# Kernel tuning notes

Hardware: AMD Instinct MI355X
Metric: run time of the kernel (lower is better)

The kernel has to match this reference:

```python
import jax, jax.numpy as jnp
import numpy as np

K_SIZE = 5      # kernel_size
NUM_ITERS = 3   # num_iters
EPS = 1e-6


def _unfold(x, k):
    """Mimic F.unfold(x, k, padding=k//2) -> (B, N, K, D) with K=k*k, N=H*W.
    Channel ordering matches torch: unfold gives (B, D*K, N) with d-major, so
    view(B, D, K, N).permute(0, 3, 2, 1) == transpose below."""
    B, D, H, W = x.shape
    p = k // 2
    xp = jnp.pad(x, ((0, 0), (0, 0), (p, p), (p, p)))
    # stack k*k shifted views -> (B, D, K, H, W); loop is over the fixed 5x5 window
    patches = jnp.stack([xp[:, :, i:i + H, j:j + W]
                         for i in range(k) for j in range(k)], axis=2)
    return patches.reshape(B, D, k * k, H * W).transpose(0, 3, 2, 1)  # (B,N,K,D)


def setup_inputs() -> dict:
    key = jax.random.key(0)
    embeddings = jax.random.normal(key, (2, 32, 256, 256), dtype=jnp.float32)
    # init_bandwidth=1.0 -> log(exp(1)-1) so softplus(log_bandwidth)=1.0
    log_bandwidth = jnp.asarray(np.log(np.exp(1.0) - 1.0), dtype=jnp.float32)
    return {"embeddings": embeddings, "log_bandwidth": log_bandwidth}


def reference(embeddings, log_bandwidth):
    B, D, H, W = embeddings.shape
    N = H * W
    z = embeddings.reshape(B, D, N).transpose(0, 2, 1)  # (B, N, D)
    bandwidth = jax.nn.softplus(log_bandwidth)
    inv_2bw2 = 1.0 / (2.0 * bandwidth * bandwidth)
    # NOTE: original code unfolds `embeddings` (not z) every iter -> constant patches
    patches = _unfold(embeddings, K_SIZE)  # (B, N, K, D)
    for _ in range(NUM_ITERS):
        z_flat = jax.lax.stop_gradient(z)  # matches z.detach()
        diff = patches - z_flat[:, :, None, :]           # (B, N, K, D)
        dist2 = jnp.sum(diff * diff, axis=-1)            # (B, N, K)
        weights = jnp.exp(-dist2 * inv_2bw2)             # gaussian kernel
        numerator = jnp.einsum('bnk,bnkd->bnd', weights, patches)
        denom = jnp.sum(weights, axis=2, keepdims=True) + EPS
        z = numerator / denom
    # default flags: only shifted embeddings are returned
    return z.transpose(0, 2, 1).reshape(B, D, H, W)
```

## Files before the change

### kernel.cpp

```cpp
#include <hip/hip_runtime.h>
#include <math.h>


typedef _Float16 h2  __attribute__((ext_vector_type(2)));
typedef _Float16 h8  __attribute__((ext_vector_type(8)));
typedef unsigned int u4v __attribute__((ext_vector_type(4)));

constexpr int Dch  = 32;
constexpr int HH   = 256;
constexpr int WW   = 256;
constexpr int PADp = 2;
constexpr int BH   = 16;
constexpr int BW   = 16;
constexpr int TH   = BH + 2 * PADp;
constexpr int TWd  = BW + 2 * PADp;
constexpr int NPIX = TH * TWd;
constexpr int NPIXP = 402;
constexpr int NCHK = 4;
constexpr int ITERS = 3;
constexpr int HWp  = HH * WW;
constexpr int NTHR = 512;

__device__ __forceinline__ float fdot2f(h2 a, h2 b, float c) {
    return __builtin_amdgcn_fdot2(a, b, c, false);
}

__device__ __forceinline__ float EXP2F(float x) {
#if __has_builtin(__builtin_amdgcn_exp2f)
    return __builtin_amdgcn_exp2f(x);
#else
    return __expf(x * 0.69314718055994531f);
#endif
}

__device__ __forceinline__ float qswap(float x) {
#if __has_builtin(__builtin_amdgcn_mov_dpp)
    return __int_as_float(
        __builtin_amdgcn_mov_dpp(__float_as_int(x), 0xB1, 0xF, 0xF, true));
#else
    return __shfl_xor(x, 1, 64);
#endif
}

__device__ __forceinline__ h2 as_h2(unsigned int x) {
    return __builtin_bit_cast(h2, x);
}

__global__ __launch_bounds__(NTHR, 4)
void meanshift_kernel(const float* __restrict__ E,
                      const float* __restrict__ lbw,
                      float* __restrict__ out)
{
    __shared__ u4v tile[NCHK][NPIXP];

    const int b    = blockIdx.z;
    const int oh   = blockIdx.y * BH - PADp;
    const int ow   = blockIdx.x * BW - PADp;
    const int tid  = threadIdx.x;
    const int half = tid & 1;
    const int pix  = tid >> 1;
    const int px   = pix & (BW - 1);
    const int py   = pix >> 4;
    const int c0   = 2 * half;

    const float bwv   = log1pf(__expf(lbw[0]));
    const float cc2   = 1.0f / (2.0f * bwv * bwv);
    const float negNC = -cc2 * 1.44269504f;

    const float* Eb = E + (size_t)b * Dch * HWp;

    for (int job = tid; job < NCHK * NPIX; job += NTHR) {
        const int cc = job / NPIX;
        const int p  = job - cc * NPIX;
        const int tr = p / TWd;
        const int tc = p - tr * TWd;
        const int gh = oh + tr;
        const int gw = ow + tc;
        h8 v;
        if ((unsigned)gh < (unsigned)HH && (unsigned)gw < (unsigned)WW) {
            const float* p0 = Eb + (size_t)(8 * cc) * HWp + gh * WW + gw;
            #pragma unroll
            for (int k = 0; k < 8; ++k) v[k] = (_Float16)p0[k * HWp];
        } else {
            #pragma unroll
            for (int k = 0; k < 8; ++k) v[k] = (_Float16)0.f;
        }
        tile[cc][p] = __builtin_bit_cast(u4v, v);
    }
    __syncthreads();

    const u4v* __restrict__ tA = tile[c0];
    const u4v* __restrict__ tB = tile[c0 + 1];

    const int myp = (py + PADp) * TWd + (px + PADp);
    h2 z0, z1, z2, z3, z4, z5, z6, z7;
    {
        const u4v ca = tA[myp];
        const u4v cb = tB[myp];
        z0 = as_h2(ca[0]); z1 = as_h2(ca[1]); z2 = as_h2(ca[2]); z3 = as_h2(ca[3]);
        z4 = as_h2(cb[0]); z5 = as_h2(cb[1]); z6 = as_h2(cb[2]); z7 = as_h2(cb[3]);
    }

    float* Ob = out + (size_t)b * Dch * HWp;
    const int off    = (oh + PADp + py) * WW + (ow + PADp + px);
    const int chbase = 16 * half;

#define NBODY(NPI) do {                                                       \
        const u4v a  = tA[(NPI)];                                             \
        const u4v bq = tB[(NPI)];                                             \
        const h2 pa0 = as_h2(a[0]),  pa1 = as_h2(a[1]);                       \
        const h2 pa2 = as_h2(a[2]),  pa3 = as_h2(a[3]);                       \
        const h2 pb0 = as_h2(bq[0]), pb1 = as_h2(bq[1]);                      \
        const h2 pb2 = as_h2(bq[2]), pb3 = as_h2(bq[3]);                      \
        const h2 e0 = pa0 - z0, e1 = pa1 - z1, e2 = pa2 - z2, e3 = pa3 - z3;  \
        const h2 f0 = pb0 - z4, f1 = pb1 - z5, f2 = pb2 - z6, f3 = pb3 - z7;  \
        float s0 = fdot2f(e0, e0, 0.f);                                       \
        s0 = fdot2f(e1, e1, s0); s0 = fdot2f(e2, e2, s0);                     \
        s0 = fdot2f(e3, e3, s0);                                              \
        float s1 = fdot2f(f0, f0, 0.f);                                       \
        s1 = fdot2f(f1, f1, s1); s1 = fdot2f(f2, f2, s1);                     \
        s1 = fdot2f(f3, f3, s1);                                              \
        const float dp   = s0 + s1;                                           \
        const float dist = dp + qswap(dp);                                    \
        const float w    = EXP2F(dist * negNC);                               \
        den += w;                                                             \
        const _Float16 wh = (_Float16)w;                                      \
        const h2 w2v = {wh, wh};                                              \
        n0 += pa0 * w2v; n1 += pa1 * w2v; n2 += pa2 * w2v; n3 += pa3 * w2v;   \
        n4 += pb0 * w2v; n5 += pb1 * w2v; n6 += pb2 * w2v; n7 += pb3 * w2v;   \
    } while (0)

    #pragma unroll 1
    for (int it = 0; it < ITERS; ++it) {
        h2 n0 = {(_Float16)0.f, (_Float16)0.f};
        h2 n1 = n0, n2 = n0, n3 = n0, n4 = n0, n5 = n0, n6 = n0, n7 = n0;
        float den = 0.f;

        #pragma unroll 1
        for (int di = 0; di < 5; ++di) {
            const int rb = (py + di) * TWd + px;
            NBODY(rb + 0);
            NBODY(rb + 1);
            NBODY(rb + 2);
            NBODY(rb + 3);
            NBODY(rb + 4);
        }

        const float invf = 1.0f / (den + 1e-6f);
        if (it == ITERS - 1) {
#define WR(IDX, NV, EL) Ob[(size_t)(chbase + (IDX)) * HWp + off] = (float)NV[EL] * invf
            WR(0,  n0, 0); WR(1,  n0, 1); WR(2,  n1, 0); WR(3,  n1, 1);
            WR(4,  n2, 0); WR(5,  n2, 1); WR(6,  n3, 0); WR(7,  n3, 1);
            WR(8,  n4, 0); WR(9,  n4, 1); WR(10, n5, 0); WR(11, n5, 1);
            WR(12, n6, 0); WR(13, n6, 1); WR(14, n7, 0); WR(15, n7, 1);
#undef WR
        } else {
            const _Float16 ih = (_Float16)invf;
            const h2 iv = {ih, ih};
            z0 = n0 * iv; z1 = n1 * iv; z2 = n2 * iv; z3 = n3 * iv;
            z4 = n4 * iv; z5 = n5 * iv; z6 = n6 * iv; z7 = n7 * iv;
        }
    }
#undef NBODY
}

extern "C" void kernel_launch(void* const* d_in, const int* in_sizes, int n_in,
                              void* d_out, int out_size, void* d_ws, size_t ws_size,
                              hipStream_t stream) {
    const float* E   = (const float*)d_in[0];
    const float* lbw = (const float*)d_in[1];
    float* out       = (float*)d_out;

    const int B = in_sizes[0] / (Dch * HWp);
    dim3 grid(WW / BW, HH / BH, B);
    dim3 block(NTHR, 1, 1);
    hipLaunchKernelGGL(meanshift_kernel, grid, block, 0, stream, E, lbw, out);
}
```

Measured before the change: 35.93 us.

## Compute two vertically adjacent pixels per thread to share LDS window reads

Each thread now handles two output pixels in the same column (rows py0 and py0+1), with the block shrunk to 256 threads. It loads each window row once from LDS into registers and reuses it for both pixels, reading 6 rows instead of 10 per pixel pair. The LDS tile is re-laid out with a padded row stride of 21 and a padded plane stride, presumably to reduce bank conflicts. The cost is roughly double the accumulator registers per thread and fewer threads per block, which lowers occupancy and wave-level parallelism.

```diff
diff --git a/kernel.cpp b/kernel.cpp
--- a/kernel.cpp
+++ b/kernel.cpp
@@ -14,12 +14,11 @@
 constexpr int BW   = 16;
 constexpr int TH   = BH + 2 * PADp;
 constexpr int TWd  = BW + 2 * PADp;
-constexpr int NPIX = TH * TWd;
-constexpr int NPIXP = 402;
-constexpr int NCHK = 4;
+constexpr int RSTR = 21;
+constexpr int PSTR = TH * RSTR + 1;
 constexpr int ITERS = 3;
 constexpr int HWp  = HH * WW;
-constexpr int NTHR = 512;
+constexpr int NTHR = 256;
 
 __device__ __forceinline__ float fdot2f(h2 a, h2 b, float c) {
     return __builtin_amdgcn_fdot2(a, b, c, false);
@@ -46,32 +45,33 @@
     return __builtin_bit_cast(h2, x);
 }
 
-__global__ __launch_bounds__(NTHR, 4)
+__global__ __launch_bounds__(NTHR, 2)
 void meanshift_kernel(const float* __restrict__ E,
                       const float* __restrict__ lbw,
                       float* __restrict__ out)
 {
-    __shared__ u4v tile[NCHK][NPIXP];
-
-    const int b    = blockIdx.z;
+    __shared__ u4v tile[4 * PSTR];
+
+    const int bz   = blockIdx.z;
     const int oh   = blockIdx.y * BH - PADp;
     const int ow   = blockIdx.x * BW - PADp;
     const int tid  = threadIdx.x;
     const int half = tid & 1;
-    const int pix  = tid >> 1;
-    const int px   = pix & (BW - 1);
-    const int py   = pix >> 4;
+    const int idx  = tid >> 1;
+    const int px   = idx & (BW - 1);
+    const int pyy  = idx >> 4;
+    const int py0  = 2 * pyy;
     const int c0   = 2 * half;
 
     const float bwv   = log1pf(__expf(lbw[0]));
     const float cc2   = 1.0f / (2.0f * bwv * bwv);
     const float negNC = -cc2 * 1.44269504f;
 
-    const float* Eb = E + (size_t)b * Dch * HWp;
-
-    for (int job = tid; job < NCHK * NPIX; job += NTHR) {
-        const int cc = job / NPIX;
-        const int p  = job - cc * NPIX;
+    const float* Eb = E + (size_t)bz * Dch * HWp;
+
+    for (int job = tid; job < 4 * (TH * TWd); job += NTHR) {
+        const int cc = job / (TH * TWd);
+        const int p  = job - cc * (TH * TWd);
         const int tr = p / TWd;
         const int tc = p - tr * TWd;
         const int gh = oh + tr;
@@ -85,35 +85,39 @@
             #pragma unroll
             for (int k = 0; k < 8; ++k) v[k] = (_Float16)0.f;
         }
-        tile[cc][p] = __builtin_bit_cast(u4v, v);
+        tile[cc * PSTR + tr * RSTR + tc] = __builtin_bit_cast(u4v, v);
     }
     __syncthreads();
 
-    const u4v* __restrict__ tA = tile[c0];
-    const u4v* __restrict__ tB = tile[c0 + 1];
-
-    const int myp = (py + PADp) * TWd + (px + PADp);
-    h2 z0, z1, z2, z3, z4, z5, z6, z7;
+    const u4v* __restrict__ tA = tile + c0 * PSTR;
+    const u4v* __restrict__ tB = tA + PSTR;
+
+    const int mypA = (py0 + 2) * RSTR + (px + 2);
+    const int mypB = mypA + RSTR;
+    h2 zA0, zA1, zA2, zA3, zA4, zA5, zA6, zA7;
+    h2 zB0, zB1, zB2, zB3, zB4, zB5, zB6, zB7;
     {
-        const u4v ca = tA[myp];
-        const u4v cb = tB[myp];
-        z0 = as_h2(ca[0]); z1 = as_h2(ca[1]); z2 = as_h2(ca[2]); z3 = as_h2(ca[3]);
-        z4 = as_h2(cb[0]); z5 = as_h2(cb[1]); z6 = as_h2(cb[2]); z7 = as_h2(cb[3]);
+        const u4v ca = tA[mypA], cb = tB[mypA];
+        zA0 = as_h2(ca[0]); zA1 = as_h2(ca[1]); zA2 = as_h2(ca[2]); zA3 = as_h2(ca[3]);
+        zA4 = as_h2(cb[0]); zA5 = as_h2(cb[1]); zA6 = as_h2(cb[2]); zA7 = as_h2(cb[3]);
+        const u4v da = tA[mypB], db = tB[mypB];
+        zB0 = as_h2(da[0]); zB1 = as_h2(da[1]); zB2 = as_h2(da[2]); zB3 = as_h2(da[3]);
+        zB4 = as_h2(db[0]); zB5 = as_h2(db[1]); zB6 = as_h2(db[2]); zB7 = as_h2(db[3]);
     }
 
-    float* Ob = out + (size_t)b * Dch * HWp;
-    const int off    = (oh + PADp + py) * WW + (ow + PADp + px);
+    float* Ob = out + (size_t)bz * Dch * HWp;
+    const int offA   = (oh + PADp + py0) * WW + (ow + PADp + px);
     const int chbase = 16 * half;
 
-#define NBODY(NPI) do {                                                       \
-        const u4v a  = tA[(NPI)];                                             \
-        const u4v bq = tB[(NPI)];                                             \
-        const h2 pa0 = as_h2(a[0]),  pa1 = as_h2(a[1]);                       \
-        const h2 pa2 = as_h2(a[2]),  pa3 = as_h2(a[3]);                       \
-        const h2 pb0 = as_h2(bq[0]), pb1 = as_h2(bq[1]);                      \
-        const h2 pb2 = as_h2(bq[2]), pb3 = as_h2(bq[3]);                      \
-        const h2 e0 = pa0 - z0, e1 = pa1 - z1, e2 = pa2 - z2, e3 = pa3 - z3;  \
-        const h2 f0 = pb0 - z4, f1 = pb1 - z5, f2 = pb2 - z6, f3 = pb3 - z7;  \
+#define NBODY(RA, RB, ZP, NP, DEN) do {                                       \
+        const h2 pa0 = as_h2(RA[0]), pa1 = as_h2(RA[1]);                      \
+        const h2 pa2 = as_h2(RA[2]), pa3 = as_h2(RA[3]);                      \
+        const h2 pb0 = as_h2(RB[0]), pb1 = as_h2(RB[1]);                      \
+        const h2 pb2 = as_h2(RB[2]), pb3 = as_h2(RB[3]);                      \
+        const h2 e0 = pa0 - ZP##0, e1 = pa1 - ZP##1;                          \
+        const h2 e2 = pa2 - ZP##2, e3 = pa3 - ZP##3;                          \
+        const h2 f0 = pb0 - ZP##4, f1 = pb1 - ZP##5;                          \
+        const h2 f2 = pb2 - ZP##6, f3 = pb3 - ZP##7;                          \
         float s0 = fdot2f(e0, e0, 0.f);                                       \
         s0 = fdot2f(e1, e1, s0); s0 = fdot2f(e2, e2, s0);                     \
         s0 = fdot2f(e3, e3, s0);                                              \
@@ -123,42 +127,76 @@
         const float dp   = s0 + s1;                                           \
         const float dist = dp + qswap(dp);                                    \
         const float w    = EXP2F(dist * negNC);                               \
-        den += w;                                                             \
+        DEN += w;                                                             \
         const _Float16 wh = (_Float16)w;                                      \
         const h2 w2v = {wh, wh};                                              \
-        n0 += pa0 * w2v; n1 += pa1 * w2v; n2 += pa2 * w2v; n3 += pa3 * w2v;   \
-        n4 += pb0 * w2v; n5 += pb1 * w2v; n6 += pb2 * w2v; n7 += pb3 * w2v;   \
+        NP##0 += pa0 * w2v; NP##1 += pa1 * w2v;                               \
+        NP##2 += pa2 * w2v; NP##3 += pa3 * w2v;                               \
+        NP##4 += pb0 * w2v; NP##5 += pb1 * w2v;                               \
+        NP##6 += pb2 * w2v; NP##7 += pb3 * w2v;                               \
     } while (0)
 
     #pragma unroll 1
     for (int it = 0; it < ITERS; ++it) {
-        h2 n0 = {(_Float16)0.f, (_Float16)0.f};
-        h2 n1 = n0, n2 = n0, n3 = n0, n4 = n0, n5 = n0, n6 = n0, n7 = n0;
-        float den = 0.f;
+        h2 nA0 = {(_Float16)0.f, (_Float16)0.f};
+        h2 nA1 = nA0, nA2 = nA0, nA3 = nA0, nA4 = nA0, nA5 = nA0, nA6 = nA0, nA7 = nA0;
+        h2 nB0 = nA0, nB1 = nA0, nB2 = nA0, nB3 = nA0, nB4 = nA0, nB5 = nA0, nB6 = nA0, nB7 = nA0;
+        float denA = 0.f, denB = 0.f;
 
         #pragma unroll 1
-        for (int di = 0; di < 5; ++di) {
-            const int rb = (py + di) * TWd + px;
-            NBODY(rb + 0);
-            NBODY(rb + 1);
-            NBODY(rb + 2);
-            NBODY(rb + 3);
-            NBODY(rb + 4);
+        for (int di = 0; di < 6; ++di) {
+            const int rwb = (py0 + di) * RSTR + px;
+            const u4v qa0 = tA[rwb + 0], qa1 = tA[rwb + 1], qa2 = tA[rwb + 2];
+            const u4v qa3 = tA[rwb + 3], qa4 = tA[rwb + 4];
+            const u4v qb0 = tB[rwb + 0], qb1 = tB[rwb + 1], qb2 = tB[rwb + 2];
+            const u4v qb3 = tB[rwb + 3], qb4 = tB[rwb + 4];
+            if (di != 5) {
+                NBODY(qa0, qb0, zA, nA, denA);
+                NBODY(qa1, qb1, zA, nA, denA);
+                NBODY(qa2, qb2, zA, nA, denA);
+                NBODY(qa3, qb3, zA, nA, denA);
+                NBODY(qa4, qb4, zA, nA, denA);
+            }
+            if (di != 0) {
+                NBODY(qa0, qb0, zB, nB, denB);
+                NBODY(qa1, qb1, zB, nB, denB);
+                NBODY(qa2, qb2, zB, nB, denB);
+                NBODY(qa3, qb3, zB, nB, denB);
+                NBODY(qa4, qb4, zB, nB, denB);
+            }
         }
 
-        const float invf = 1.0f / (den + 1e-6f);
+        const float invA = 1.0f / (denA + 1e-6f);
+        const float invB = 1.0f / (denB + 1e-6f);
         if (it == ITERS - 1) {
-#define WR(IDX, NV, EL) Ob[(size_t)(chbase + (IDX)) * HWp + off] = (float)NV[EL] * invf
-            WR(0,  n0, 0); WR(1,  n0, 1); WR(2,  n1, 0); WR(3,  n1, 1);
-            WR(4,  n2, 0); WR(5,  n2, 1); WR(6,  n3, 0); WR(7,  n3, 1);
-            WR(8,  n4, 0); WR(9,  n4, 1); WR(10, n5, 0); WR(11, n5, 1);
-            WR(12, n6, 0); WR(13, n6, 1); WR(14, n7, 0); WR(15, n7, 1);
+#define WR(IDX, NV, EL, OFF, INV) \
+            Ob[(size_t)(chbase + (IDX)) * HWp + (OFF)] = (float)NV[EL] * (INV)
+            WR(0,  nA0, 0, offA, invA); WR(1,  nA0, 1, offA, invA);
+            WR(2,  nA1, 0, offA, invA); WR(3,  nA1, 1, offA, invA);
+            WR(4,  nA2, 0, offA, invA); WR(5,  nA2, 1, offA, invA);
+            WR(6,  nA3, 0, offA, invA); WR(7,  nA3, 1, offA, invA);
+            WR(8,  nA4, 0, offA, invA); WR(9,  nA4, 1, offA, invA);
+            WR(10, nA5, 0, offA, invA); WR(11, nA5, 1, offA, invA);
+            WR(12, nA6, 0, offA, invA); WR(13, nA6, 1, offA, invA);
+            WR(14, nA7, 0, offA, invA); WR(15, nA7, 1, offA, invA);
+            WR(0,  nB0, 0, offA + WW, invB); WR(1,  nB0, 1, offA + WW, invB);
+            WR(2,  nB1, 0, offA + WW, invB); WR(3,  nB1, 1, offA + WW, invB);
+            WR(4,  nB2, 0, offA + WW, invB); WR(5,  nB2, 1, offA + WW, invB);
+            WR(6,  nB3, 0, offA + WW, invB); WR(7,  nB3, 1, offA + WW, invB);
+            WR(8,  nB4, 0, offA + WW, invB); WR(9,  nB4, 1, offA + WW, invB);
+            WR(10, nB5, 0, offA + WW, invB); WR(11, nB5, 1, offA + WW, invB);
+            WR(12, nB6, 0, offA + WW, invB); WR(13, nB6, 1, offA + WW, invB);
+            WR(14, nB7, 0, offA + WW, invB); WR(15, nB7, 1, offA + WW, invB);
 #undef WR
         } else {
-            const _Float16 ih = (_Float16)invf;
-            const h2 iv = {ih, ih};
-            z0 = n0 * iv; z1 = n1 * iv; z2 = n2 * iv; z3 = n3 * iv;
-            z4 = n4 * iv; z5 = n5 * iv; z6 = n6 * iv; z7 = n7 * iv;
+            const _Float16 ihA = (_Float16)invA;
+            const _Float16 ihB = (_Float16)invB;
+            const h2 ivA = {ihA, ihA};
+            const h2 ivB = {ihB, ihB};
+            zA0 = nA0 * ivA; zA1 = nA1 * ivA; zA2 = nA2 * ivA; zA3 = nA3 * ivA;
+            zA4 = nA4 * ivA; zA5 = nA5 * ivA; zA6 = nA6 * ivA; zA7 = nA7 * ivA;
+            zB0 = nB0 * ivB; zB1 = nB1 * ivB; zB2 = nB2 * ivB; zB3 = nB3 * ivB;
+            zB4 = nB4 * ivB; zB5 = nB5 * ivB; zB6 = nB6 * ivB; zB7 = nB7 * ivB;
         }
     }
 #undef NBODY
```

New measurement: 37.98 us. +5.7%, slower.

## Split channels across four lanes per pixel with padded LDS rows

Applied to the files above, without the earlier changes.

Each pixel is now handled by four lanes, each owning 8 channels, instead of two lanes with 16. Partial distances are reduced with two DPP swaps. The block tile shrinks to 8x16 pixels, and the LDS row stride is padded to 21 to reduce bank conflicts. The five window loads per row are hoisted ahead of the compute. This gives more parallelism and smaller per-thread register state, allowing 8 blocks per CU, at the cost of a larger halo overhead per tile and an extra cross-lane reduction step.

```diff
diff --git a/kernel.cpp b/kernel.cpp
--- a/kernel.cpp
+++ b/kernel.cpp
@@ -10,13 +10,12 @@
 constexpr int HH   = 256;
 constexpr int WW   = 256;
 constexpr int PADp = 2;
-constexpr int BH   = 16;
+constexpr int BH   = 8;
 constexpr int BW   = 16;
 constexpr int TH   = BH + 2 * PADp;
 constexpr int TWd  = BW + 2 * PADp;
-constexpr int NPIX = TH * TWd;
-constexpr int NPIXP = 402;
-constexpr int NCHK = 4;
+constexpr int RSTR = 21;
+constexpr int PSTR = TH * RSTR + 1;
 constexpr int ITERS = 3;
 constexpr int HWp  = HH * WW;
 constexpr int NTHR = 512;
@@ -33,45 +32,44 @@
 #endif
 }
 
-__device__ __forceinline__ float qswap(float x) {
-#if __has_builtin(__builtin_amdgcn_mov_dpp)
+__device__ __forceinline__ float qswap1(float x) {
     return __int_as_float(
         __builtin_amdgcn_mov_dpp(__float_as_int(x), 0xB1, 0xF, 0xF, true));
-#else
-    return __shfl_xor(x, 1, 64);
-#endif
+}
+__device__ __forceinline__ float qswap2(float x) {
+    return __int_as_float(
+        __builtin_amdgcn_mov_dpp(__float_as_int(x), 0x4E, 0xF, 0xF, true));
 }
 
 __device__ __forceinline__ h2 as_h2(unsigned int x) {
     return __builtin_bit_cast(h2, x);
 }
 
-__global__ __launch_bounds__(NTHR, 4)
+__global__ __launch_bounds__(NTHR, 8)
 void meanshift_kernel(const float* __restrict__ E,
                       const float* __restrict__ lbw,
                       float* __restrict__ out)
 {
-    __shared__ u4v tile[NCHK][NPIXP];
+    __shared__ u4v tile[4 * PSTR];
 
-    const int b    = blockIdx.z;
-    const int oh   = blockIdx.y * BH - PADp;
-    const int ow   = blockIdx.x * BW - PADp;
-    const int tid  = threadIdx.x;
-    const int half = tid & 1;
-    const int pix  = tid >> 1;
-    const int px   = pix & (BW - 1);
-    const int py   = pix >> 4;
-    const int c0   = 2 * half;
+    const int bz  = blockIdx.z;
+    const int oh  = blockIdx.y * BH - PADp;
+    const int ow  = blockIdx.x * BW - PADp;
+    const int tid = threadIdx.x;
+    const int cq  = tid & 3;
+    const int idx = tid >> 2;
+    const int px  = idx & (BW - 1);
+    const int py  = idx >> 4;
 
     const float bwv   = log1pf(__expf(lbw[0]));
     const float cc2   = 1.0f / (2.0f * bwv * bwv);
     const float negNC = -cc2 * 1.44269504f;
 
-    const float* Eb = E + (size_t)b * Dch * HWp;
+    const float* Eb = E + (size_t)bz * Dch * HWp;
 
-    for (int job = tid; job < NCHK * NPIX; job += NTHR) {
-        const int cc = job / NPIX;
-        const int p  = job - cc * NPIX;
+    for (int job = tid; job < 4 * (TH * TWd); job += NTHR) {
+        const int cc = job / (TH * TWd);
+        const int p  = job - cc * (TH * TWd);
         const int tr = p / TWd;
         const int tc = p - tr * TWd;
         const int gh = oh + tr;
@@ -85,80 +83,74 @@
             #pragma unroll
             for (int k = 0; k < 8; ++k) v[k] = (_Float16)0.f;
         }
-        tile[cc][p] = __builtin_bit_cast(u4v, v);
+        tile[cc * PSTR + tr * RSTR + tc] = __builtin_bit_cast(u4v, v);
     }
     __syncthreads();
 
-    const u4v* __restrict__ tA = tile[c0];
-    const u4v* __restrict__ tB = tile[c0 + 1];
+    const u4v* __restrict__ tP = tile + cq * PSTR;
 
-    const int myp = (py + PADp) * TWd + (px + PADp);
-    h2 z0, z1, z2, z3, z4, z5, z6, z7;
+    h2 z0, z1, z2, z3;
     {
-        const u4v ca = tA[myp];
-        const u4v cb = tB[myp];
-        z0 = as_h2(ca[0]); z1 = as_h2(ca[1]); z2 = as_h2(ca[2]); z3 = as_h2(ca[3]);
-        z4 = as_h2(cb[0]); z5 = as_h2(cb[1]); z6 = as_h2(cb[2]); z7 = as_h2(cb[3]);
+        const u4v ca = tP[(py + 2) * RSTR + (px + 2)];
+        z0 = as_h2(ca[0]); z1 = as_h2(ca[1]);
+        z2 = as_h2(ca[2]); z3 = as_h2(ca[3]);
     }
 
-    float* Ob = out + (size_t)b * Dch * HWp;
+    float* Ob = out + (size_t)bz * Dch * HWp;
     const int off    = (oh + PADp + py) * WW + (ow + PADp + px);
-    const int chbase = 16 * half;
+    const int chbase = 8 * cq;
 
-#define NBODY(NPI) do {                                                       \
-        const u4v a  = tA[(NPI)];                                             \
-        const u4v bq = tB[(NPI)];                                             \
-        const h2 pa0 = as_h2(a[0]),  pa1 = as_h2(a[1]);                       \
-        const h2 pa2 = as_h2(a[2]),  pa3 = as_h2(a[3]);                       \
-        const h2 pb0 = as_h2(bq[0]), pb1 = as_h2(bq[1]);                      \
-        const h2 pb2 = as_h2(bq[2]), pb3 = as_h2(bq[3]);                      \
-        const h2 e0 = pa0 - z0, e1 = pa1 - z1, e2 = pa2 - z2, e3 = pa3 - z3;  \
-        const h2 f0 = pb0 - z4, f1 = pb1 - z5, f2 = pb2 - z6, f3 = pb3 - z7;  \
+#define NBODY(Q) do {                                                         \
+        const h2 p0 = as_h2(Q[0]), p1 = as_h2(Q[1]);                          \
+        const h2 p2 = as_h2(Q[2]), p3 = as_h2(Q[3]);                          \
+        const h2 e0 = p0 - z0, e1 = p1 - z1;                                  \
+        const h2 e2 = p2 - z2, e3 = p3 - z3;                                  \
         float s0 = fdot2f(e0, e0, 0.f);                                       \
-        s0 = fdot2f(e1, e1, s0); s0 = fdot2f(e2, e2, s0);                     \
-        s0 = fdot2f(e3, e3, s0);                                              \
-        float s1 = fdot2f(f0, f0, 0.f);                                       \
-        s1 = fdot2f(f1, f1, s1); s1 = fdot2f(f2, f2, s1);                     \
-        s1 = fdot2f(f3, f3, s1);                                              \
-        const float dp   = s0 + s1;                                           \
-        const float dist = dp + qswap(dp);                                    \
-        const float w    = EXP2F(dist * negNC);                               \
+        float s1 = fdot2f(e1, e1, 0.f);                                       \
+        s0 = fdot2f(e2, e2, s0);                                              \
+        s1 = fdot2f(e3, e3, s1);                                              \
+        const float dp = s0 + s1;                          \
+        const float d2 = dp + qswap1(dp);                                     \
+        const float dist = d2 + qswap2(d2);             \
+        const float w = EXP2F(dist * negNC);                                  \
         den += w;                                                             \
         const _Float16 wh = (_Float16)w;                                      \
         const h2 w2v = {wh, wh};                                              \
-        n0 += pa0 * w2v; n1 += pa1 * w2v; n2 += pa2 * w2v; n3 += pa3 * w2v;   \
-        n4 += pb0 * w2v; n5 += pb1 * w2v; n6 += pb2 * w2v; n7 += pb3 * w2v;   \
+        n0 += p0 * w2v; n1 += p1 * w2v;                                       \
+        n2 += p2 * w2v; n3 += p3 * w2v;                                       \
     } while (0)
 
     #pragma unroll 1
     for (int it = 0; it < ITERS; ++it) {
         h2 n0 = {(_Float16)0.f, (_Float16)0.f};
-        h2 n1 = n0, n2 = n0, n3 = n0, n4 = n0, n5 = n0, n6 = n0, n7 = n0;
+        h2 n1 = n0, n2 = n0, n3 = n0;
         float den = 0.f;
 
         #pragma unroll 1
         for (int di = 0; di < 5; ++di) {
-            const int rb = (py + di) * TWd + px;
-            NBODY(rb + 0);
-            NBODY(rb + 1);
-            NBODY(rb + 2);
-            NBODY(rb + 3);
-            NBODY(rb + 4);
+            const int rwb = (py + di) * RSTR + px;
+            const u4v q0 = tP[rwb + 0];
+            const u4v q1 = tP[rwb + 1];
+            const u4v q2 = tP[rwb + 2];
+            const u4v q3 = tP[rwb + 3];
+            const u4v q4 = tP[rwb + 4];
+            NBODY(q0);
+            NBODY(q1);
+            NBODY(q2);
+            NBODY(q3);
+            NBODY(q4);
         }
 
         const float invf = 1.0f / (den + 1e-6f);
         if (it == ITERS - 1) {
 #define WR(IDX, NV, EL) Ob[(size_t)(chbase + (IDX)) * HWp + off] = (float)NV[EL] * invf
-            WR(0,  n0, 0); WR(1,  n0, 1); WR(2,  n1, 0); WR(3,  n1, 1);
-            WR(4,  n2, 0); WR(5,  n2, 1); WR(6,  n3, 0); WR(7,  n3, 1);
-            WR(8,  n4, 0); WR(9,  n4, 1); WR(10, n5, 0); WR(11, n5, 1);
-            WR(12, n6, 0); WR(13, n6, 1); WR(14, n7, 0); WR(15, n7, 1);
+            WR(0, n0, 0); WR(1, n0, 1); WR(2, n1, 0); WR(3, n1, 1);
+            WR(4, n2, 0); WR(5, n2, 1); WR(6, n3, 0); WR(7, n3, 1);
 #undef WR
         } else {
             const _Float16 ih = (_Float16)invf;
             const h2 iv = {ih, ih};
             z0 = n0 * iv; z1 = n1 * iv; z2 = n2 * iv; z3 = n3 * iv;
-            z4 = n4 * iv; z5 = n5 * iv; z6 = n6 * iv; z7 = n7 * iv;
         }
     }
 #undef NBODY
```

New measurement: 38.30 us. 1.07x slower.

## Expand squared distance into precomputed norms plus scaled dot product

Applied to the files above, without the earlier changes.

Rewrites ||p−z||² as ||p||² − 2p·z + ||z||², folding the bandwidth scale into each term. Each tile pixel's squared norm is computed once into shared memory, and the 25 neighbor values are held in registers. z is pre-scaled so each neighbor needs only fdot2 accumulations seeded with the precomputed terms, which removes the packed half subtractions and the final scaling multiply. The 5x5 loop is fully unrolled and fp16 packing uses cvt_pkrtz. The trade-offs are higher register pressure under the 64-VGPR launch bound and some fp16 cancellation risk in the expanded form.

```diff
diff --git a/kernel.cpp b/kernel.cpp
--- a/kernel.cpp
+++ b/kernel.cpp
@@ -46,14 +46,23 @@
     return __builtin_bit_cast(h2, x);
 }
 
+__device__ __forceinline__ h2 pk2(float a, float b) {
+#if __has_builtin(__builtin_amdgcn_cvt_pkrtz)
+    return __builtin_bit_cast(h2, __builtin_amdgcn_cvt_pkrtz(a, b));
+#else
+    h2 r; r[0] = (_Float16)a; r[1] = (_Float16)b; return r;
+#endif
+}
+
 __global__ __launch_bounds__(NTHR, 4)
 void meanshift_kernel(const float* __restrict__ E,
                       const float* __restrict__ lbw,
                       float* __restrict__ out)
 {
-    __shared__ u4v tile[NCHK][NPIXP];
-
-    const int b    = blockIdx.z;
+    __shared__ u4v  tile[NCHK][NPIXP];
+    __shared__ float sqv[NPIX];
+
+    const int bz   = blockIdx.z;
     const int oh   = blockIdx.y * BH - PADp;
     const int ow   = blockIdx.x * BW - PADp;
     const int tid  = threadIdx.x;
@@ -63,11 +72,13 @@
     const int py   = pix >> 4;
     const int c0   = 2 * half;
 
-    const float bwv   = log1pf(__expf(lbw[0]));
-    const float cc2   = 1.0f / (2.0f * bwv * bwv);
-    const float negNC = -cc2 * 1.44269504f;
-
-    const float* Eb = E + (size_t)b * Dch * HWp;
+    const float bwv = log1pf(__expf(lbw[0]));
+    const float cc2 = 1.0f / (2.0f * bwv * bwv);
+    const float NCf = cc2 * 1.44269504f;
+    const float A2f = 2.0f * NCf;
+    const float MZC = -1.0f / (8.0f * NCf);
+
+    const float* Eb = E + (size_t)bz * Dch * HWp;
 
     for (int job = tid; job < NCHK * NPIX; job += NTHR) {
         const int cc = job / NPIX;
@@ -89,62 +100,96 @@
     }
     __syncthreads();
 
+    for (int p = tid; p < NPIX; p += NTHR) {
+        const u4v t0 = tile[0][p], t1 = tile[1][p];
+        const u4v t2 = tile[2][p], t3 = tile[3][p];
+        float a0 = 0.f, a1 = 0.f, a2 = 0.f, a3 = 0.f;
+        #pragma unroll
+        for (int j = 0; j < 4; ++j) {
+            const h2 q0 = as_h2(t0[j]); a0 = fdot2f(q0, q0, a0);
+            const h2 q1 = as_h2(t1[j]); a1 = fdot2f(q1, q1, a1);
+            const h2 q2 = as_h2(t2[j]); a2 = fdot2f(q2, q2, a2);
+            const h2 q3 = as_h2(t3[j]); a3 = fdot2f(q3, q3, a3);
+        }
+        sqv[p] = -0.5f * NCf * ((a0 + a1) + (a2 + a3));
+    }
+    __syncthreads();
+
     const u4v* __restrict__ tA = tile[c0];
     const u4v* __restrict__ tB = tile[c0 + 1];
 
-    const int myp = (py + PADp) * TWd + (px + PADp);
-    h2 z0, z1, z2, z3, z4, z5, z6, z7;
+    const int rb0 = (py + 0) * TWd + px;
+    const int rb1 = (py + 1) * TWd + px;
+    const int rb2 = (py + 2) * TWd + px;
+    const int rb3 = (py + 3) * TWd + px;
+    const int rb4 = (py + 4) * TWd + px;
+    const float S00 = sqv[rb0+0], S01 = sqv[rb0+1], S02 = sqv[rb0+2], S03 = sqv[rb0+3], S04 = sqv[rb0+4];
+    const float S10 = sqv[rb1+0], S11 = sqv[rb1+1], S12 = sqv[rb1+2], S13 = sqv[rb1+3], S14 = sqv[rb1+4];
+    const float S20 = sqv[rb2+0], S21 = sqv[rb2+1], S22 = sqv[rb2+2], S23 = sqv[rb2+3], S24 = sqv[rb2+4];
+    const float S30 = sqv[rb3+0], S31 = sqv[rb3+1], S32 = sqv[rb3+2], S33 = sqv[rb3+3], S34 = sqv[rb3+4];
+    const float S40 = sqv[rb4+0], S41 = sqv[rb4+1], S42 = sqv[rb4+2], S43 = sqv[rb4+3], S44 = sqv[rb4+4];
+
+    h2 zs0, zs1, zs2, zs3, zs4, zs5, zs6, zs7;
     {
+        const int myp = rb2 + 2;
         const u4v ca = tA[myp];
         const u4v cb = tB[myp];
-        z0 = as_h2(ca[0]); z1 = as_h2(ca[1]); z2 = as_h2(ca[2]); z3 = as_h2(ca[3]);
-        z4 = as_h2(cb[0]); z5 = as_h2(cb[1]); z6 = as_h2(cb[2]); z7 = as_h2(cb[3]);
-    }
-
-    float* Ob = out + (size_t)b * Dch * HWp;
+        const h2 A2v = pk2(A2f, A2f);
+        zs0 = as_h2(ca[0]) * A2v; zs1 = as_h2(ca[1]) * A2v;
+        zs2 = as_h2(ca[2]) * A2v; zs3 = as_h2(ca[3]) * A2v;
+        zs4 = as_h2(cb[0]) * A2v; zs5 = as_h2(cb[1]) * A2v;
+        zs6 = as_h2(cb[2]) * A2v; zs7 = as_h2(cb[3]) * A2v;
+    }
+
+    float* Ob = out + (size_t)bz * Dch * HWp;
     const int off    = (oh + PADp + py) * WW + (ow + PADp + px);
     const int chbase = 16 * half;
 
-#define NBODY(NPI) do {                                                       \
+#define NBODY(NPI, HS) do {                                                   \
         const u4v a  = tA[(NPI)];                                             \
         const u4v bq = tB[(NPI)];                                             \
         const h2 pa0 = as_h2(a[0]),  pa1 = as_h2(a[1]);                       \
         const h2 pa2 = as_h2(a[2]),  pa3 = as_h2(a[3]);                       \
         const h2 pb0 = as_h2(bq[0]), pb1 = as_h2(bq[1]);                      \
         const h2 pb2 = as_h2(bq[2]), pb3 = as_h2(bq[3]);                      \
-        const h2 e0 = pa0 - z0, e1 = pa1 - z1, e2 = pa2 - z2, e3 = pa3 - z3;  \
-        const h2 f0 = pb0 - z4, f1 = pb1 - z5, f2 = pb2 - z6, f3 = pb3 - z7;  \
-        float s0 = fdot2f(e0, e0, 0.f);                                       \
-        s0 = fdot2f(e1, e1, s0); s0 = fdot2f(e2, e2, s0);                     \
-        s0 = fdot2f(e3, e3, s0);                                              \
-        float s1 = fdot2f(f0, f0, 0.f);                                       \
-        s1 = fdot2f(f1, f1, s1); s1 = fdot2f(f2, f2, s1);                     \
-        s1 = fdot2f(f3, f3, s1);                                              \
-        const float dp   = s0 + s1;                                           \
-        const float dist = dp + qswap(dp);                                    \
-        const float w    = EXP2F(dist * negNC);                               \
+        float s0 = fdot2f(pa0, zs0, (HS));                                    \
+        s0 = fdot2f(pa1, zs1, s0); s0 = fdot2f(pa2, zs2, s0);                 \
+        s0 = fdot2f(pa3, zs3, s0);                                            \
+        float s1 = fdot2f(pb0, zs4, mzz);                                     \
+        s1 = fdot2f(pb1, zs5, s1); s1 = fdot2f(pb2, zs6, s1);                 \
+        s1 = fdot2f(pb3, zs7, s1);                                            \
+        const float dp  = s0 + s1;                                            \
+        const float arg = dp + qswap(dp);   \
+        const float w   = EXP2F(arg);                              \
         den += w;                                                             \
-        const _Float16 wh = (_Float16)w;                                      \
-        const h2 w2v = {wh, wh};                                              \
+        const h2 w2v = pk2(w, w);                                             \
         n0 += pa0 * w2v; n1 += pa1 * w2v; n2 += pa2 * w2v; n3 += pa3 * w2v;   \
         n4 += pb0 * w2v; n5 += pb1 * w2v; n6 += pb2 * w2v; n7 += pb3 * w2v;   \
     } while (0)
 
     #pragma unroll 1
     for (int it = 0; it < ITERS; ++it) {
+        float mzz;
+        {
+            float q0 = fdot2f(zs0, zs0, 0.f);
+            q0 = fdot2f(zs1, zs1, q0); q0 = fdot2f(zs2, zs2, q0);
+            q0 = fdot2f(zs3, zs3, q0);
+            float q1 = fdot2f(zs4, zs4, 0.f);
+            q1 = fdot2f(zs5, zs5, q1); q1 = fdot2f(zs6, zs6, q1);
+            q1 = fdot2f(zs7, zs7, q1);
+            const float qs = q0 + q1;
+            mzz = (qs + qswap(qs)) * MZC;
+        }
+
         h2 n0 = {(_Float16)0.f, (_Float16)0.f};
         h2 n1 = n0, n2 = n0, n3 = n0, n4 = n0, n5 = n0, n6 = n0, n7 = n0;
         float den = 0.f;
 
-        #pragma unroll 1
-        for (int di = 0; di < 5; ++di) {
-            const int rb = (py + di) * TWd + px;
-            NBODY(rb + 0);
-            NBODY(rb + 1);
-            NBODY(rb + 2);
-            NBODY(rb + 3);
-            NBODY(rb + 4);
-        }
+        NBODY(rb0+0, S00); NBODY(rb0+1, S01); NBODY(rb0+2, S02); NBODY(rb0+3, S03); NBODY(rb0+4, S04);
+        NBODY(rb1+0, S10); NBODY(rb1+1, S11); NBODY(rb1+2, S12); NBODY(rb1+3, S13); NBODY(rb1+4, S14);
+        NBODY(rb2+0, S20); NBODY(rb2+1, S21); NBODY(rb2+2, S22); NBODY(rb2+3, S23); NBODY(rb2+4, S24);
+        NBODY(rb3+0, S30); NBODY(rb3+1, S31); NBODY(rb3+2, S32); NBODY(rb3+3, S33); NBODY(rb3+4, S34);
+        NBODY(rb4+0, S40); NBODY(rb4+1, S41); NBODY(rb4+2, S42); NBODY(rb4+3, S43); NBODY(rb4+4, S44);
 
         const float invf = 1.0f / (den + 1e-6f);
         if (it == ITERS - 1) {
@@ -155,10 +200,10 @@
             WR(12, n6, 0); WR(13, n6, 1); WR(14, n7, 0); WR(15, n7, 1);
 #undef WR
         } else {
-            const _Float16 ih = (_Float16)invf;
-            const h2 iv = {ih, ih};
-            z0 = n0 * iv; z1 = n1 * iv; z2 = n2 * iv; z3 = n3 * iv;
-            z4 = n4 * iv; z5 = n5 * iv; z6 = n6 * iv; z7 = n7 * iv;
+            const float ia = invf * A2f;
+            const h2 iv = pk2(ia, ia);
+            zs0 = n0 * iv; zs1 = n1 * iv; zs2 = n2 * iv; zs3 = n3 * iv;
+            zs4 = n4 * iv; zs5 = n5 * iv; zs6 = n6 * iv; zs7 = n7 * iv;
         }
     }
 #undef NBODY
```

New measurement: 109.9 us. +205.8%, slower.
